# Optimization experiments

Hardware: AMD Instinct MI355X
Metric: run time of the kernel (lower is better)

Reference implementation:

```python
import jax, jax.numpy as jnp
import numpy as np

B, C, T = 1024, 64, 275
S = 10            # number of subjects
EMB = 184         # encoder embedding dim
PROJ = 1024       # projector dim
LN_EPS = 1e-5


def setup_inputs() -> dict:
    key = jax.random.key(0)
    ks = jax.random.split(key, 12)
    sc = lambda *shape: 1.0 / np.sqrt(shape[-1] if len(shape) > 1 else 1.0)
    return {
        "eeg": jax.random.normal(ks[0], (B, C, T), dtype=jnp.float32),
        "subject_ids": jax.random.randint(ks[1], (B,), 0, S, dtype=jnp.int64),
        # per-subject Linear(T, T): y = x @ W.T + b
        "subj_W": jax.random.normal(ks[2], (S, T, T), dtype=jnp.float32) / np.sqrt(T),
        "subj_b": jax.random.normal(ks[3], (S, T), dtype=jnp.float32) * 0.02,
        # encoder stub: flatten (C*T) -> Linear -> EMB
        "enc_W": jax.random.normal(ks[4], (C * T, EMB), dtype=jnp.float32) / np.sqrt(C * T),
        "enc_b": jnp.zeros((EMB,), dtype=jnp.float32),
        # projector: Linear(EMB, PROJ) -> ResidualAdd(GELU -> Linear(PROJ, PROJ)) -> LayerNorm
        "W1": jax.random.normal(ks[5], (EMB, PROJ), dtype=jnp.float32) / np.sqrt(EMB),
        "b1": jnp.zeros((PROJ,), dtype=jnp.float32),
        "W2": jax.random.normal(ks[6], (PROJ, PROJ), dtype=jnp.float32) / np.sqrt(PROJ),
        "b2": jnp.zeros((PROJ,), dtype=jnp.float32),
        "gamma": jnp.ones((PROJ,), dtype=jnp.float32),
        "beta": jnp.zeros((PROJ,), dtype=jnp.float32),
    }


def reference(eeg, subject_ids, subj_W, subj_b, enc_W, enc_b, W1, b1, W2, b2, gamma, beta):
    # --- subject-wise alignment: grouped gather -> linear -> scatter ---
    # Vectorized form of the per-subject loop: each row b uses weight subj_W[sid[b]].
    Wg = subj_W[subject_ids]              # [B, T, T]
    bg = subj_b[subject_ids]              # [B, T]
    # torch Linear: y = x @ W.T + b  ->  y[b,c,u] = sum_t eeg[b,c,t] * Wg[b,u,t]
    x = jnp.einsum("bct,but->bcu", eeg, Wg) + bg[:, None, :]   # [B, C, T]

    # --- encoder stub (SpatioTemporalCNN placeholder): flatten + linear ---
    h = x.reshape(x.shape[0], -1) @ enc_W + enc_b              # [B, EMB]

    # --- MLPProjector ---
    h = h @ W1 + b1                                            # [B, PROJ]
    r = jax.nn.gelu(h, approximate=False) @ W2 + b2            # dropout is identity at eval
    h = h + r
    # LayerNorm over last dim
    mu = jnp.mean(h, axis=-1, keepdims=True)
    var = jnp.mean(jnp.square(h - mu), axis=-1, keepdims=True)
    out = (h - mu) * jax.lax.rsqrt(var + LN_EPS) * gamma + beta
    return out
```

## Files before the change

### kernel.cpp

```cpp
#include <hip/hip_runtime.h>
#include <math.h>

#define B_N    1024
#define C_N    64
#define T_N    275
#define S_N    10
#define EMB_N  184
#define PROJ_N 1024
#define CT_N   (C_N * T_N)
#define TP     288
#define TPAD   296
#define KP2    18432
#define EMBP   192
#define KZ2    32
#define KC2    (KP2 / KZ2)
#define KZ5    2

typedef unsigned short u16;
typedef __attribute__((ext_vector_type(8))) short short8;
typedef __attribute__((ext_vector_type(4))) short short4v;
typedef __attribute__((ext_vector_type(4))) float f32x4;

#define MFMA16(a,b,c) __builtin_amdgcn_mfma_f32_16x16x32_bf16(a, b, c, 0, 0, 0)

__device__ __forceinline__ u16 f2bf(float f) {
    union { float f; unsigned u; } v; v.f = f;
    unsigned r = v.u + 0x7FFFu + ((v.u >> 16) & 1u);
    return (u16)(r >> 16);
}
__device__ __forceinline__ float gelu_exact(float v) {
    return 0.5f * v * (1.0f + erff(v * 0.70710678118654752f));
}
__device__ __forceinline__ void gload16(const void* g, void* lds) {
    __builtin_amdgcn_global_load_lds(
        (const __attribute__((address_space(1))) void*)g,
        (__attribute__((address_space(3))) void*)lds, 16, 0, 0);
}

__global__ __launch_bounds__(256) void p_eeg(const float* __restrict__ eeg,
                                             u16* __restrict__ eegb)
{
    const int b = blockIdx.x;
    const float* src = eeg + (size_t)b * CT_N;
    u16* dst = eegb + (size_t)b * C_N * TPAD;
    for (int o4 = threadIdx.x; o4 < C_N * TPAD / 4; o4 += 256) {
        int o = o4 * 4;
        int r = o / TPAD, tt = o - r * TPAD;
        short4v pk;
        #pragma unroll
        for (int e = 0; e < 4; ++e) {
            int t = tt + e;
            float v = (t < T_N) ? src[r * T_N + t] : 0.f;
            pk[e] = (short)f2bf(v);
        }
        *reinterpret_cast<short4v*>(dst + o) = pk;
    }
}

__global__ __launch_bounds__(256) void p_wbf16(const float* __restrict__ W,
                                               u16* __restrict__ Wb)
{
    int idx4 = blockIdx.x * 256 + threadIdx.x;
    if (idx4 >= S_N * TP * TPAD / 4) return;
    int o = idx4 * 4;
    int row = o / TPAD, tt = o - row * TPAD;
    int s = row / TP, u = row - s * TP;
    short4v pk;
    #pragma unroll
    for (int e = 0; e < 4; ++e) {
        int t = tt + e;
        float v = (u < T_N && t < T_N) ? W[((size_t)s * T_N + u) * T_N + t] : 0.f;
        pk[e] = (short)f2bf(v);
    }
    *reinterpret_cast<short4v*>(Wb + o) = pk;
}

__global__ __launch_bounds__(256) void p_encwt(const float* __restrict__ encW,
                                               u16* __restrict__ eT)
{
    __shared__ float tile[64][65];
    const int t = blockIdx.x;
    const int n0 = blockIdx.y * 64;
    const int tid = threadIdx.x;
    const int j = tid & 63, cg = tid >> 6;
    #pragma unroll
    for (int pass = 0; pass < 16; ++pass) {
        int c = pass * 4 + cg;
        float v = 0.f;
        if (t < T_N && n0 + j < EMB_N)
            v = encW[((size_t)c * T_N + t) * EMB_N + n0 + j];
        tile[c][j] = v;
    }
    __syncthreads();
    #pragma unroll
    for (int pass = 0; pass < 16; ++pass) {
        int nl = pass * 4 + cg;
        eT[(size_t)(n0 + nl) * KP2 + t * 64 + j] = f2bf(tile[j][nl]);
    }
}

__global__ __launch_bounds__(256) void p_w1t(const float* __restrict__ W1,
                                             u16* __restrict__ w1t)
{
    __shared__ float tile[64][65];
    const int k0 = blockIdx.x * 64, n0 = blockIdx.y * 64;
    for (int l = threadIdx.x; l < 4096; l += 256) {
        int i = l >> 6, j = l & 63;
        float v = (k0 + i < EMB_N) ? W1[(size_t)(k0 + i) * PROJ_N + n0 + j] : 0.f;
        tile[i][j] = v;
    }
    __syncthreads();
    for (int l = threadIdx.x; l < 4096; l += 256) {
        int j = l >> 6, i = l & 63;
        w1t[(size_t)(n0 + j) * EMBP + k0 + i] = f2bf(tile[i][j]);
    }
}

__global__ __launch_bounds__(256) void p_w2t(const float* __restrict__ W2,
                                             u16* __restrict__ w2t)
{
    __shared__ float tile[64][65];
    const int k0 = blockIdx.x * 64, n0 = blockIdx.y * 64;
    for (int l = threadIdx.x; l < 4096; l += 256) {
        int i = l >> 6, j = l & 63;
        tile[i][j] = W2[(size_t)(k0 + i) * PROJ_N + n0 + j];
    }
    __syncthreads();
    for (int l = threadIdx.x; l < 4096; l += 256) {
        int j = l >> 6, i = l & 63;
        w2t[(size_t)(n0 + j) * PROJ_N + k0 + i] = f2bf(tile[i][j]);
    }
}

__global__ __launch_bounds__(256) void k1_mfma(
    const u16* __restrict__ eegb, const int* __restrict__ sid,
    const u16* __restrict__ Wb, const float* __restrict__ subj_b,
    u16* __restrict__ xb)
{
    const int b = blockIdx.x;
    const int s = sid[b];
    const int tid = threadIdx.x;
    const int w = tid >> 6, lane = tid & 63;
    const int wr = w >> 1, wc = w & 1;
    const int lrow = lane & 15, lk = lane >> 4;
    const u16* A = eegb + (size_t)b * C_N * TPAD;
    const u16* Wr = Wb + (size_t)s * TP * TPAD;

    f32x4 acc[2][9] = {};
    for (int ks = 0; ks < 9; ++ks) {
        const int t0 = ks * 32 + 8 * lk;
        short8 af0 = *reinterpret_cast<const short8*>(A + (32 * wr + lrow) * TPAD + t0);
        short8 af1 = *reinterpret_cast<const short8*>(A + (32 * wr + 16 + lrow) * TPAD + t0);
        #pragma unroll
        for (int ct = 0; ct < 9; ++ct) {
            int u = 144 * wc + 16 * ct + lrow;
            short8 bf = *reinterpret_cast<const short8*>(Wr + (size_t)u * TPAD + t0);
            acc[0][ct] = MFMA16(af0, bf, acc[0][ct]);
            acc[1][ct] = MFMA16(af1, bf, acc[1][ct]);
        }
    }
    #pragma unroll
    for (int ct = 0; ct < 9; ++ct) {
        int u = 144 * wc + 16 * ct + lrow;
        float bias = (u < T_N) ? subj_b[s * T_N + u] : 0.f;
        bool valid = (u < T_N);
        #pragma unroll
        for (int rt = 0; rt < 2; ++rt) {
            int c0 = 32 * wr + 16 * rt + 4 * lk;
            short4v pk;
            #pragma unroll
            for (int r = 0; r < 4; ++r)
                pk[r] = valid ? (short)f2bf(acc[rt][ct][r] + bias) : (short)0;
            *reinterpret_cast<short4v*>(xb + ((size_t)b * TP + u) * C_N + c0) = pk;
        }
    }
}

__global__ __launch_bounds__(256) void k2_mfma(
    const u16* __restrict__ xb, const u16* __restrict__ eT,
    float* __restrict__ part)
{
    __shared__ u16 Abuf[2][64 * 64];
    const int m0 = blockIdx.x * 64;
    const int kz = blockIdx.y;
    const int tid = threadIdx.x;
    const int w = tid >> 6, lane = tid & 63;
    const int lrow = lane & 15, lk = lane >> 4;
    const int kbase = kz * KC2;

    const int r0 = tid >> 3, q0 = tid & 7;
    const int r1 = (tid + 256) >> 3, q1 = tid & 7;
    const u16* a0 = xb + (size_t)(m0 + r0) * KP2 + (q0 ^ (r0 & 7)) * 8;
    const u16* a1 = xb + (size_t)(m0 + r1) * KP2 + (q1 ^ (r1 & 7)) * 8;

    f32x4 acc[4][3] = {};
    int buf = 0;

    gload16(a0 + kbase, &Abuf[0][(size_t)(w * 64) * 8]);
    gload16(a1 + kbase, &Abuf[0][(size_t)(w * 64 + 256) * 8]);
    __syncthreads();

    for (int step = 0; step < 9; ++step) {
        if (step < 8) {
            int k0 = kbase + (step + 1) * 64;
            gload16(a0 + k0, &Abuf[buf ^ 1][(size_t)(w * 64) * 8]);
            gload16(a1 + k0, &Abuf[buf ^ 1][(size_t)(w * 64 + 256) * 8]);
        }
        short8 bf[3][2];
        #pragma unroll
        for (int ct = 0; ct < 3; ++ct)
            #pragma unroll
            for (int ki = 0; ki < 2; ++ki)
                bf[ct][ki] = *reinterpret_cast<const short8*>(
                    eT + (size_t)(48 * w + 16 * ct + lrow) * KP2 + kbase + step * 64 + ki * 32 + 8 * lk);
        #pragma unroll
        for (int rt = 0; rt < 4; ++rt) {
            int c = 16 * rt + lrow;
            #pragma unroll
            for (int ki = 0; ki < 2; ++ki) {
                short8 af = *reinterpret_cast<const short8*>(
                    &Abuf[buf][c * 64 + (((lk + 4 * ki) ^ (c & 7)) * 8)]);
                #pragma unroll
                for (int ct = 0; ct < 3; ++ct)
                    acc[rt][ct] = MFMA16(af, bf[ct][ki], acc[rt][ct]);
            }
        }
        __syncthreads();
        buf ^= 1;
    }

    #pragma unroll
    for (int rt = 0; rt < 4; ++rt)
        #pragma unroll
        for (int ct = 0; ct < 3; ++ct) {
            int n = 48 * w + 16 * ct + lrow;
            #pragma unroll
            for (int r = 0; r < 4; ++r) {
                int m = m0 + 16 * rt + 4 * lk + r;
                part[((size_t)kz * B_N + m) * EMBP + n] = acc[rt][ct][r];
            }
        }
}

__global__ __launch_bounds__(256) void k3_reduce(
    const float* __restrict__ part, const float* __restrict__ enc_b,
    u16* __restrict__ hb)
{
    int idx = blockIdx.x * 256 + threadIdx.x;
    if (idx >= B_N * EMBP) return;
    int n = idx % EMBP;
    float s = 0.f;
    if (n < EMB_N) {
        s = enc_b[n];
        #pragma unroll
        for (int z = 0; z < KZ2; ++z)
            s += part[(size_t)z * B_N * EMBP + idx];
    }
    hb[idx] = f2bf(s);
}

__global__ __launch_bounds__(256) void k4_mfma(
    const u16* __restrict__ hb, const u16* __restrict__ w1t,
    const float* __restrict__ b1, float* __restrict__ h1, u16* __restrict__ g)
{
    __shared__ u16 Ab[64 * EMBP];
    __shared__ u16 Bb[64 * EMBP];
    const int m0 = blockIdx.x * 64, n0 = blockIdx.y * 64;
    const int tid = threadIdx.x;
    const int w = tid >> 6, lane = tid & 63;
    const int wr = w >> 1, wc = w & 1;
    const int lrow = lane & 15, lk = lane >> 4;

    #pragma unroll
    for (int i = 0; i < 6; ++i) {
        int L = tid + i * 256;
        int row = L / 24, qp = L % 24;
        int ql = qp ^ (row & 7);
        gload16(hb  + (size_t)(m0 + row) * EMBP + ql * 8, &Ab[(size_t)(w * 64 + i * 256) * 8]);
        gload16(w1t + (size_t)(n0 + row) * EMBP + ql * 8, &Bb[(size_t)(w * 64 + i * 256) * 8]);
    }
    __syncthreads();

    f32x4 acc[2][2] = {};
    #pragma unroll
    for (int ks = 0; ks < 6; ++ks) {
        #pragma unroll
        for (int rt = 0; rt < 2; ++rt) {
            int c = 32 * wr + 16 * rt + lrow;
            short8 af = *reinterpret_cast<const short8*>(
                &Ab[c * EMBP + (((4 * ks + lk) ^ (c & 7)) * 8)]);
            #pragma unroll
            for (int ct = 0; ct < 2; ++ct) {
                int nl = 32 * wc + 16 * ct + lrow;
                short8 bfv = *reinterpret_cast<const short8*>(
                    &Bb[nl * EMBP + (((4 * ks + lk) ^ (nl & 7)) * 8)]);
                acc[rt][ct] = MFMA16(af, bfv, acc[rt][ct]);
            }
        }
    }
    #pragma unroll
    for (int rt = 0; rt < 2; ++rt)
        #pragma unroll
        for (int ct = 0; ct < 2; ++ct) {
            int n = n0 + 32 * wc + 16 * ct + lrow;
            #pragma unroll
            for (int r = 0; r < 4; ++r) {
                int m = m0 + 32 * wr + 16 * rt + 4 * lk + r;
                float v = acc[rt][ct][r] + b1[n];
                size_t o = (size_t)m * PROJ_N + n;
                h1[o] = v;
                g[o] = f2bf(gelu_exact(v));
            }
        }
}

__global__ __launch_bounds__(256) void k5_mfma(
    const u16* __restrict__ g, const u16* __restrict__ w2t,
    float* __restrict__ part2)
{
    __shared__ u16 Ab[2][64 * 64];
    __shared__ u16 Bb[2][64 * 64];
    const int m0 = blockIdx.x * 64, n0 = blockIdx.y * 64;
    const int kz = blockIdx.z;
    const int kbase = kz * (PROJ_N / KZ5);
    const int tid = threadIdx.x;
    const int w = tid >> 6, lane = tid & 63;
    const int wr = w >> 1, wc = w & 1;
    const int lrow = lane & 15, lk = lane >> 4;

    const int r0 = tid >> 3, q0 = tid & 7;
    const int r1 = (tid + 256) >> 3;
    const u16* a0 = g + (size_t)(m0 + r0) * PROJ_N + (q0 ^ (r0 & 7)) * 8;
    const u16* a1 = g + (size_t)(m0 + r1) * PROJ_N + (q0 ^ (r1 & 7)) * 8;
    const u16* b0 = w2t + (size_t)(n0 + r0) * PROJ_N + (q0 ^ (r0 & 7)) * 8;
    const u16* b1p = w2t + (size_t)(n0 + r1) * PROJ_N + (q0 ^ (r1 & 7)) * 8;

    f32x4 acc[2][2] = {};
    int buf = 0;
    gload16(a0 + kbase, &Ab[0][(size_t)(w * 64) * 8]);
    gload16(a1 + kbase, &Ab[0][(size_t)(w * 64 + 256) * 8]);
    gload16(b0 + kbase, &Bb[0][(size_t)(w * 64) * 8]);
    gload16(b1p + kbase, &Bb[0][(size_t)(w * 64 + 256) * 8]);
    __syncthreads();

    for (int step = 0; step < 8; ++step) {
        if (step < 7) {
            int k0 = kbase + (step + 1) * 64;
            gload16(a0 + k0, &Ab[buf ^ 1][(size_t)(w * 64) * 8]);
            gload16(a1 + k0, &Ab[buf ^ 1][(size_t)(w * 64 + 256) * 8]);
            gload16(b0 + k0, &Bb[buf ^ 1][(size_t)(w * 64) * 8]);
            gload16(b1p + k0, &Bb[buf ^ 1][(size_t)(w * 64 + 256) * 8]);
        }
        #pragma unroll
        for (int ki = 0; ki < 2; ++ki) {
            #pragma unroll
            for (int rt = 0; rt < 2; ++rt) {
                int c = 32 * wr + 16 * rt + lrow;
                short8 af = *reinterpret_cast<const short8*>(
                    &Ab[buf][c * 64 + (((lk + 4 * ki) ^ (c & 7)) * 8)]);
                #pragma unroll
                for (int ct = 0; ct < 2; ++ct) {
                    int nl = 32 * wc + 16 * ct + lrow;
                    short8 bfv = *reinterpret_cast<const short8*>(
                        &Bb[buf][nl * 64 + (((lk + 4 * ki) ^ (nl & 7)) * 8)]);
                    acc[rt][ct] = MFMA16(af, bfv, acc[rt][ct]);
                }
            }
        }
        __syncthreads();
        buf ^= 1;
    }
    #pragma unroll
    for (int rt = 0; rt < 2; ++rt)
        #pragma unroll
        for (int ct = 0; ct < 2; ++ct) {
            int n = n0 + 32 * wc + 16 * ct + lrow;
            #pragma unroll
            for (int r = 0; r < 4; ++r) {
                int m = m0 + 32 * wr + 16 * rt + 4 * lk + r;
                part2[(size_t)kz * B_N * PROJ_N + (size_t)m * PROJ_N + n] = acc[rt][ct][r];
            }
        }
}

__global__ __launch_bounds__(256) void k5r_ln(
    const float* __restrict__ part2, const float* __restrict__ h1,
    const float* __restrict__ b2, const float* __restrict__ gamma,
    const float* __restrict__ beta, float* __restrict__ out)
{
    const int m = blockIdx.x;
    const int tid = threadIdx.x;
    const float4* h4 = reinterpret_cast<const float4*>(h1 + (size_t)m * PROJ_N);
    const float4* p0 = reinterpret_cast<const float4*>(part2 + (size_t)m * PROJ_N);
    const float4* p1 = reinterpret_cast<const float4*>(part2 + (size_t)(B_N + m) * PROJ_N);
    const float4* b4 = reinterpret_cast<const float4*>(b2);
    float4 va = h4[tid], vb = p0[tid], vc = p1[tid], vd = b4[tid];
    float v[4] = { va.x + vb.x + vc.x + vd.x, va.y + vb.y + vc.y + vd.y,
                   va.z + vb.z + vc.z + vd.z, va.w + vb.w + vc.w + vd.w };
    float s = 0.f, sq = 0.f;
    #pragma unroll
    for (int i = 0; i < 4; ++i) { s += v[i]; sq += v[i] * v[i]; }
    #pragma unroll
    for (int off = 32; off > 0; off >>= 1) {
        s  += __shfl_down(s, off);
        sq += __shfl_down(sq, off);
    }
    __shared__ float ss[4], ssq[4];
    int wid = tid >> 6, lane = tid & 63;
    if (lane == 0) { ss[wid] = s; ssq[wid] = sq; }
    __syncthreads();
    if (tid == 0) {
        float a = 0.f, bsum = 0.f;
        #pragma unroll
        for (int q = 0; q < 4; ++q) { a += ss[q]; bsum += ssq[q]; }
        ss[0] = a; ssq[0] = bsum;
    }
    __syncthreads();
    float mu  = ss[0] * (1.0f / PROJ_N);
    float var = ssq[0] * (1.0f / PROJ_N) - mu * mu;
    float rs  = rsqrtf(var + 1e-5f);
    const float4 g4 = reinterpret_cast<const float4*>(gamma)[tid];
    const float4 be4 = reinterpret_cast<const float4*>(beta)[tid];
    float gg[4] = { g4.x, g4.y, g4.z, g4.w };
    float bb[4] = { be4.x, be4.y, be4.z, be4.w };
    float4 o4;
    float* op = reinterpret_cast<float*>(&o4);
    #pragma unroll
    for (int i = 0; i < 4; ++i) op[i] = (v[i] - mu) * rs * gg[i] + bb[i];
    reinterpret_cast<float4*>(out + (size_t)m * PROJ_N)[tid] = o4;
}

extern "C" void kernel_launch(void* const* d_in, const int* in_sizes, int n_in,
                              void* d_out, int out_size, void* d_ws, size_t ws_size,
                              hipStream_t stream)
{
    const float* eeg    = (const float*)d_in[0];
    const int*   sid    = (const int*)  d_in[1];
    const float* subj_W = (const float*)d_in[2];
    const float* subj_b = (const float*)d_in[3];
    const float* enc_W  = (const float*)d_in[4];
    const float* enc_b  = (const float*)d_in[5];
    const float* W1     = (const float*)d_in[6];
    const float* b1     = (const float*)d_in[7];
    const float* W2     = (const float*)d_in[8];
    const float* b2     = (const float*)d_in[9];
    const float* gamma  = (const float*)d_in[10];
    const float* beta   = (const float*)d_in[11];
    float* out = (float*)d_out;

    char* w = (char*)d_ws;
    u16*   xb    = (u16*)(w);
    u16*   Wb    = (u16*)(w + 37748736);
    u16*   eT    = (u16*)(w + 39453696);
    u16*   w1t   = (u16*)(w + 46531584);
    u16*   w2t   = (u16*)(w + 46924800);
    u16*   hb    = (u16*)(w + 49021952);
    float* h1    = (float*)(w + 49415168);
    u16*   g     = (u16*)(w + 53609472);
    char*  scr   = w + 55706624;
    u16*   eegb  = (u16*)scr;
    float* part  = (float*)scr;
    float* part2 = (float*)(scr + 25165824);

    p_eeg   <<<dim3(B_N), 256, 0, stream>>>(eeg, eegb);
    p_wbf16 <<<dim3((S_N * TP * TPAD / 4 + 255) / 256), 256, 0, stream>>>(subj_W, Wb);
    p_encwt <<<dim3(TP, 3), 256, 0, stream>>>(enc_W, eT);
    p_w1t   <<<dim3(EMBP / 64, PROJ_N / 64), 256, 0, stream>>>(W1, w1t);
    p_w2t   <<<dim3(PROJ_N / 64, PROJ_N / 64), 256, 0, stream>>>(W2, w2t);

    k1_mfma <<<dim3(B_N), 256, 0, stream>>>(eegb, sid, Wb, subj_b, xb);
    k2_mfma <<<dim3(16, KZ2), 256, 0, stream>>>(xb, eT, part);
    k3_reduce<<<dim3((B_N * EMBP + 255) / 256), 256, 0, stream>>>(part, enc_b, hb);
    k4_mfma <<<dim3(16, 16), 256, 0, stream>>>(hb, w1t, b1, h1, g);
    k5_mfma <<<dim3(16, 16, KZ5), 256, 0, stream>>>(g, w2t, part2);
    k5r_ln  <<<dim3(B_N), 256, 0, stream>>>(part2, h1, b2, gamma, beta, out);
}
```

Before: 143.2 us.

## Fuse prep kernels, group batches by subject in k1, enlarge k2 tile

Merges the five preprocessing kernels into one launch and adds a block that buckets batch rows by subject id into groups of four. The subject-wise GEMM then processes four same-subject rows per 512-thread block, staging the shared subject weight in double-buffered LDS so it is reused across rows. The encoder GEMM tile grows to 128 rows with register prefetch of the B operand, and the TPAD padding is removed. These changes aim to cut launch overhead and redundant weight traffic, in exchange for more registers, padded groups that do no useful work, and a serial prefix computation inside the fused prep kernel.

After: 132.2 us. 1.08x faster.

```diff
diff --git a/kernel.cpp b/kernel.cpp
--- a/kernel.cpp
+++ b/kernel.cpp
@@ -9,12 +9,12 @@
 #define PROJ_N 1024
 #define CT_N   (C_N * T_N)
 #define TP     288
-#define TPAD   296
-#define KP2    18432
+#define KP2    (TP * C_N)
 #define EMBP   192
 #define KZ2    32
 #define KC2    (KP2 / KZ2)
 #define KZ5    2
+#define GMAX   264
 
 typedef unsigned short u16;
 typedef __attribute__((ext_vector_type(8))) short short8;
@@ -37,200 +37,290 @@
         (__attribute__((address_space(3))) void*)lds, 16, 0, 0);
 }
 
-__global__ __launch_bounds__(256) void p_eeg(const float* __restrict__ eeg,
-                                             u16* __restrict__ eegb)
-{
-    const int b = blockIdx.x;
-    const float* src = eeg + (size_t)b * CT_N;
-    u16* dst = eegb + (size_t)b * C_N * TPAD;
-    for (int o4 = threadIdx.x; o4 < C_N * TPAD / 4; o4 += 256) {
-        int o = o4 * 4;
-        int r = o / TPAD, tt = o - r * TPAD;
+__global__ __launch_bounds__(256) void p_all(
+    const float* __restrict__ eeg, const int* __restrict__ sid,
+    const float* __restrict__ W, const float* __restrict__ encW,
+    const float* __restrict__ W1, const float* __restrict__ W2,
+    u16* __restrict__ eegb, u16* __restrict__ Wb, u16* __restrict__ eT,
+    u16* __restrict__ w1t, u16* __restrict__ w2t, int* __restrict__ bsq)
+{
+    __shared__ char smem[16640];
+    const int blk = blockIdx.x;
+    const int tid = threadIdx.x;
+
+    if (blk < 1024) {
+        const int b = blk;
+        const float* src = eeg + (size_t)b * CT_N;
+        u16* dst = eegb + (size_t)b * C_N * TP;
+        #pragma unroll
+        for (int p = 0; p < 9; ++p) {
+            int ch = tid + p * 256;
+            int c = ch / 36, q8 = ch - c * 36;
+            int t0 = q8 * 8;
+            short8 pk;
+            #pragma unroll
+            for (int e = 0; e < 8; ++e) {
+                int t = t0 + e;
+                float v = (t < T_N) ? src[c * T_N + t] : 0.f;
+                pk[e] = (short)f2bf(v);
+            }
+            *reinterpret_cast<short8*>(dst + c * TP + t0) = pk;
+        }
+        return;
+    }
+    if (blk < 1834) {
+        int idx4 = (blk - 1024) * 256 + tid;
+        if (idx4 >= S_N * TP * TP / 4) return;
+        int o = idx4 * 4;
+        int row = o / TP, t = o - row * TP;
+        int s = row / TP, u = row - s * TP;
         short4v pk;
         #pragma unroll
         for (int e = 0; e < 4; ++e) {
-            int t = tt + e;
-            float v = (t < T_N) ? src[r * T_N + t] : 0.f;
+            float v = (u < T_N && t + e < T_N)
+                ? W[((size_t)s * T_N + u) * T_N + t + e] : 0.f;
             pk[e] = (short)f2bf(v);
         }
-        *reinterpret_cast<short4v*>(dst + o) = pk;
-    }
-}
-
-__global__ __launch_bounds__(256) void p_wbf16(const float* __restrict__ W,
-                                               u16* __restrict__ Wb)
-{
-    int idx4 = blockIdx.x * 256 + threadIdx.x;
-    if (idx4 >= S_N * TP * TPAD / 4) return;
-    int o = idx4 * 4;
-    int row = o / TPAD, tt = o - row * TPAD;
-    int s = row / TP, u = row - s * TP;
-    short4v pk;
-    #pragma unroll
-    for (int e = 0; e < 4; ++e) {
-        int t = tt + e;
-        float v = (u < T_N && t < T_N) ? W[((size_t)s * T_N + u) * T_N + t] : 0.f;
-        pk[e] = (short)f2bf(v);
-    }
-    *reinterpret_cast<short4v*>(Wb + o) = pk;
-}
-
-__global__ __launch_bounds__(256) void p_encwt(const float* __restrict__ encW,
-                                               u16* __restrict__ eT)
-{
-    __shared__ float tile[64][65];
-    const int t = blockIdx.x;
-    const int n0 = blockIdx.y * 64;
-    const int tid = threadIdx.x;
-    const int j = tid & 63, cg = tid >> 6;
-    #pragma unroll
-    for (int pass = 0; pass < 16; ++pass) {
-        int c = pass * 4 + cg;
-        float v = 0.f;
-        if (t < T_N && n0 + j < EMB_N)
-            v = encW[((size_t)c * T_N + t) * EMB_N + n0 + j];
-        tile[c][j] = v;
-    }
-    __syncthreads();
-    #pragma unroll
-    for (int pass = 0; pass < 16; ++pass) {
-        int nl = pass * 4 + cg;
-        eT[(size_t)(n0 + nl) * KP2 + t * 64 + j] = f2bf(tile[j][nl]);
-    }
-}
-
-__global__ __launch_bounds__(256) void p_w1t(const float* __restrict__ W1,
-                                             u16* __restrict__ w1t)
-{
-    __shared__ float tile[64][65];
-    const int k0 = blockIdx.x * 64, n0 = blockIdx.y * 64;
-    for (int l = threadIdx.x; l < 4096; l += 256) {
-        int i = l >> 6, j = l & 63;
-        float v = (k0 + i < EMB_N) ? W1[(size_t)(k0 + i) * PROJ_N + n0 + j] : 0.f;
-        tile[i][j] = v;
-    }
-    __syncthreads();
-    for (int l = threadIdx.x; l < 4096; l += 256) {
-        int j = l >> 6, i = l & 63;
-        w1t[(size_t)(n0 + j) * EMBP + k0 + i] = f2bf(tile[i][j]);
-    }
-}
-
-__global__ __launch_bounds__(256) void p_w2t(const float* __restrict__ W2,
-                                             u16* __restrict__ w2t)
-{
-    __shared__ float tile[64][65];
-    const int k0 = blockIdx.x * 64, n0 = blockIdx.y * 64;
-    for (int l = threadIdx.x; l < 4096; l += 256) {
-        int i = l >> 6, j = l & 63;
-        tile[i][j] = W2[(size_t)(k0 + i) * PROJ_N + n0 + j];
-    }
-    __syncthreads();
-    for (int l = threadIdx.x; l < 4096; l += 256) {
-        int j = l >> 6, i = l & 63;
-        w2t[(size_t)(n0 + j) * PROJ_N + k0 + i] = f2bf(tile[i][j]);
-    }
-}
-
-__global__ __launch_bounds__(256) void k1_mfma(
+        *reinterpret_cast<short4v*>(Wb + o) = pk;
+        return;
+    }
+    if (blk < 2698) {
+        float (*tile)[65] = (float(*)[65])smem;
+        int local = blk - 1834;
+        const int t = local / 3;
+        const int n0 = (local % 3) * 64;
+        const int j = tid & 63, cg = tid >> 6;
+        #pragma unroll
+        for (int pass = 0; pass < 16; ++pass) {
+            int c = pass * 4 + cg;
+            float v = 0.f;
+            if (t < T_N && n0 + j < EMB_N)
+                v = encW[((size_t)c * T_N + t) * EMB_N + n0 + j];
+            tile[c][j] = v;
+        }
+        __syncthreads();
+        #pragma unroll
+        for (int pass = 0; pass < 16; ++pass) {
+            int nl = pass * 4 + cg;
+            eT[(size_t)(n0 + nl) * KP2 + t * 64 + j] = f2bf(tile[j][nl]);
+        }
+        return;
+    }
+    if (blk < 2746) {
+        float (*tile)[65] = (float(*)[65])smem;
+        int local = blk - 2698;
+        const int k0 = (local % 3) * 64, n0 = (local / 3) * 64;
+        for (int l = tid; l < 4096; l += 256) {
+            int i = l >> 6, j = l & 63;
+            float v = (k0 + i < EMB_N) ? W1[(size_t)(k0 + i) * PROJ_N + n0 + j] : 0.f;
+            tile[i][j] = v;
+        }
+        __syncthreads();
+        for (int l = tid; l < 4096; l += 256) {
+            int j = l >> 6, i = l & 63;
+            w1t[(size_t)(n0 + j) * EMBP + k0 + i] = f2bf(tile[i][j]);
+        }
+        return;
+    }
+    if (blk < 3002) {
+        float (*tile)[65] = (float(*)[65])smem;
+        int local = blk - 2746;
+        const int k0 = (local % 16) * 64, n0 = (local / 16) * 64;
+        for (int l = tid; l < 4096; l += 256) {
+            int i = l >> 6, j = l & 63;
+            tile[i][j] = W2[(size_t)(k0 + i) * PROJ_N + n0 + j];
+        }
+        __syncthreads();
+        for (int l = tid; l < 4096; l += 256) {
+            int j = l >> 6, i = l & 63;
+            w2t[(size_t)(n0 + j) * PROJ_N + k0 + i] = f2bf(tile[i][j]);
+        }
+        return;
+    }
+    {
+        int* sgrp = (int*)smem;
+        int* C    = (int*)(smem + 4096);
+        int* tot  = (int*)(smem + 4096 + 640);
+        for (int i = tid; i < 1024; i += 256) sgrp[i] = sid[i];
+        for (int i = tid; i < 4 * GMAX; i += 256) bsq[i] = -1;
+        __syncthreads();
+        const int w4 = tid >> 6, lane = tid & 63;
+        #pragma unroll
+        for (int j = 0; j < 4; ++j) {
+            int chunk = w4 * 4 + j;
+            int sb = sgrp[chunk * 64 + lane];
+            int myc = 0;
+            for (int s = 0; s < S_N; ++s) {
+                unsigned long long m = __ballot(sb == s);
+                if (lane == s) myc = (int)__popcll(m);
+            }
+            if (lane < S_N) C[chunk * S_N + lane] = myc;
+        }
+        __syncthreads();
+        if (tid < S_N) {
+            int a = 0;
+            for (int w2 = 0; w2 < 16; ++w2) a += C[w2 * S_N + tid];
+            tot[tid] = a;
+        }
+        __syncthreads();
+        #pragma unroll
+        for (int rep = 0; rep < 4; ++rep) {
+            int b = tid + rep * 256;
+            int s = sgrp[b];
+            int off = 0;
+            for (int s2 = 0; s2 < S_N; ++s2)
+                if (s2 < s) off += (tot[s2] + 3) & ~3;
+            int chunk = b >> 6;
+            int rank = 0;
+            for (int w2 = 0; w2 < 16; ++w2)
+                if (w2 < chunk) rank += C[w2 * S_N + s];
+            for (int i = chunk * 64; i < b; ++i) rank += (sgrp[i] == s) ? 1 : 0;
+            bsq[off + rank] = b;
+        }
+    }
+}
+
+__global__ __launch_bounds__(512, 2) void k1g(
     const u16* __restrict__ eegb, const int* __restrict__ sid,
     const u16* __restrict__ Wb, const float* __restrict__ subj_b,
-    u16* __restrict__ xb)
-{
-    const int b = blockIdx.x;
-    const int s = sid[b];
+    const int* __restrict__ bsq, u16* __restrict__ xb)
+{
+    __shared__ u16 Bs[2][TP * 4 * 8];
+    const int g = blockIdx.x;
+    const int b0 = bsq[g * 4];
+    if (b0 < 0) return;
+    const int s = sid[b0];
     const int tid = threadIdx.x;
     const int w = tid >> 6, lane = tid & 63;
-    const int wr = w >> 1, wc = w & 1;
+    const int bi = w >> 1, uh = w & 1;
     const int lrow = lane & 15, lk = lane >> 4;
-    const u16* A = eegb + (size_t)b * C_N * TPAD;
-    const u16* Wr = Wb + (size_t)s * TP * TPAD;
-
-    f32x4 acc[2][9] = {};
+    const int b = bsq[g * 4 + bi];
+    const int bsafe = (b >= 0) ? b : 0;
+    const u16* A = eegb + (size_t)bsafe * C_N * TP;
+    const u16* Wr = Wb + (size_t)s * TP * TP;
+
+    #define K1_STAGE(st, ks)                                                   \
+        for (int l = tid; l < TP * 4; l += 512) {                              \
+            int u_ = l >> 2, q_ = l & 3;                                       \
+            gload16(Wr + (size_t)u_ * TP + (ks) * 32 + ((q_ ^ ((u_ >> 1) & 3)) << 3), \
+                    &Bs[st][l * 8]);                                           \
+        }
+
+    f32x4 acc[4][9] = {};
+    short8 a[4], an[4];
+
+    K1_STAGE(0, 0);
+    #pragma unroll
+    for (int rt = 0; rt < 4; ++rt)
+        a[rt] = *reinterpret_cast<const short8*>(A + (16 * rt + lrow) * TP + 8 * lk);
+    __syncthreads();
+
     for (int ks = 0; ks < 9; ++ks) {
-        const int t0 = ks * 32 + 8 * lk;
-        short8 af0 = *reinterpret_cast<const short8*>(A + (32 * wr + lrow) * TPAD + t0);
-        short8 af1 = *reinterpret_cast<const short8*>(A + (32 * wr + 16 + lrow) * TPAD + t0);
+        const int st = ks & 1;
+        if (ks < 8) {
+            K1_STAGE(st ^ 1, ks + 1);
+            #pragma unroll
+            for (int rt = 0; rt < 4; ++rt)
+                an[rt] = *reinterpret_cast<const short8*>(
+                    A + (16 * rt + lrow) * TP + (ks + 1) * 32 + 8 * lk);
+        }
         #pragma unroll
         for (int ct = 0; ct < 9; ++ct) {
-            int u = 144 * wc + 16 * ct + lrow;
-            short8 bf = *reinterpret_cast<const short8*>(Wr + (size_t)u * TPAD + t0);
-            acc[0][ct] = MFMA16(af0, bf, acc[0][ct]);
-            acc[1][ct] = MFMA16(af1, bf, acc[1][ct]);
-        }
-    }
+            int u = uh * 144 + 16 * ct + lrow;
+            int chunk = u * 4 + (lk ^ ((u >> 1) & 3));
+            short8 bv = *reinterpret_cast<const short8*>(&Bs[st][chunk * 8]);
+            #pragma unroll
+            for (int rt = 0; rt < 4; ++rt)
+                acc[rt][ct] = MFMA16(a[rt], bv, acc[rt][ct]);
+        }
+        __syncthreads();
+        #pragma unroll
+        for (int rt = 0; rt < 4; ++rt) a[rt] = an[rt];
+    }
+
+    if (b < 0) return;
     #pragma unroll
     for (int ct = 0; ct < 9; ++ct) {
-        int u = 144 * wc + 16 * ct + lrow;
-        float bias = (u < T_N) ? subj_b[s * T_N + u] : 0.f;
-        bool valid = (u < T_N);
-        #pragma unroll
-        for (int rt = 0; rt < 2; ++rt) {
-            int c0 = 32 * wr + 16 * rt + 4 * lk;
+        int u = uh * 144 + 16 * ct + lrow;
+        if (u >= T_N) continue;
+        float bias = subj_b[s * T_N + u];
+        #pragma unroll
+        for (int rt = 0; rt < 4; ++rt) {
+            int c0 = 16 * rt + 4 * lk;
             short4v pk;
             #pragma unroll
             for (int r = 0; r < 4; ++r)
-                pk[r] = valid ? (short)f2bf(acc[rt][ct][r] + bias) : (short)0;
+                pk[r] = (short)f2bf(acc[rt][ct][r] + bias);
             *reinterpret_cast<short4v*>(xb + ((size_t)b * TP + u) * C_N + c0) = pk;
         }
     }
+    #undef K1_STAGE
 }
 
 __global__ __launch_bounds__(256) void k2_mfma(
     const u16* __restrict__ xb, const u16* __restrict__ eT,
     float* __restrict__ part)
 {
-    __shared__ u16 Abuf[2][64 * 64];
-    const int m0 = blockIdx.x * 64;
+    __shared__ u16 Ab[2][128 * 64];
+    const int m0 = blockIdx.x * 128;
     const int kz = blockIdx.y;
+    const int kbase = kz * KC2;
     const int tid = threadIdx.x;
     const int w = tid >> 6, lane = tid & 63;
     const int lrow = lane & 15, lk = lane >> 4;
-    const int kbase = kz * KC2;
-
-    const int r0 = tid >> 3, q0 = tid & 7;
-    const int r1 = (tid + 256) >> 3, q1 = tid & 7;
-    const u16* a0 = xb + (size_t)(m0 + r0) * KP2 + (q0 ^ (r0 & 7)) * 8;
-    const u16* a1 = xb + (size_t)(m0 + r1) * KP2 + (q1 ^ (r1 & 7)) * 8;
-
-    f32x4 acc[4][3] = {};
-    int buf = 0;
-
-    gload16(a0 + kbase, &Abuf[0][(size_t)(w * 64) * 8]);
-    gload16(a1 + kbase, &Abuf[0][(size_t)(w * 64 + 256) * 8]);
+
+    #define K2_STAGE(st, step)                                                 \
+        _Pragma("unroll")                                                      \
+        for (int p = 0; p < 4; ++p) {                                          \
+            int l = tid + p * 256;                                             \
+            int r_ = l >> 3, q_ = l & 7;                                       \
+            gload16(xb + (size_t)(m0 + r_) * KP2 + kbase + (step) * 64 +       \
+                        ((q_ ^ (r_ & 7)) << 3),                                \
+                    &Ab[st][l * 8]);                                           \
+        }
+
+    #define K2_BLOAD(step, dst)                                                \
+        _Pragma("unroll")                                                      \
+        for (int ct = 0; ct < 3; ++ct)                                         \
+            _Pragma("unroll")                                                  \
+            for (int ki = 0; ki < 2; ++ki)                                     \
+                dst[ct][ki] = *reinterpret_cast<const short8*>(                \
+                    eT + (size_t)(48 * w + 16 * ct + lrow) * KP2 + kbase +     \
+                    (step) * 64 + ki * 32 + 8 * lk);
+
+    f32x4 acc[8][3] = {};
+    short8 bf[3][2], bn[3][2];
+
+    K2_STAGE(0, 0);
+    K2_BLOAD(0, bf);
     __syncthreads();
 
     for (int step = 0; step < 9; ++step) {
+        const int st = step & 1;
         if (step < 8) {
-            int k0 = kbase + (step + 1) * 64;
-            gload16(a0 + k0, &Abuf[buf ^ 1][(size_t)(w * 64) * 8]);
-            gload16(a1 + k0, &Abuf[buf ^ 1][(size_t)(w * 64 + 256) * 8]);
-        }
-        short8 bf[3][2];
-        #pragma unroll
-        for (int ct = 0; ct < 3; ++ct)
-            #pragma unroll
-            for (int ki = 0; ki < 2; ++ki)
-                bf[ct][ki] = *reinterpret_cast<const short8*>(
-                    eT + (size_t)(48 * w + 16 * ct + lrow) * KP2 + kbase + step * 64 + ki * 32 + 8 * lk);
-        #pragma unroll
-        for (int rt = 0; rt < 4; ++rt) {
-            int c = 16 * rt + lrow;
-            #pragma unroll
-            for (int ki = 0; ki < 2; ++ki) {
-                short8 af = *reinterpret_cast<const short8*>(
-                    &Abuf[buf][c * 64 + (((lk + 4 * ki) ^ (c & 7)) * 8)]);
+            K2_STAGE(st ^ 1, step + 1);
+            K2_BLOAD(step + 1, bn);
+        }
+        #pragma unroll
+        for (int ki = 0; ki < 2; ++ki)
+            #pragma unroll
+            for (int rt = 0; rt < 8; ++rt) {
+                int m = 16 * rt + lrow;
+                int chunk = m * 8 + ((4 * ki + lk) ^ (m & 7));
+                short8 af = *reinterpret_cast<const short8*>(&Ab[st][chunk * 8]);
                 #pragma unroll
                 for (int ct = 0; ct < 3; ++ct)
                     acc[rt][ct] = MFMA16(af, bf[ct][ki], acc[rt][ct]);
             }
-        }
-        __syncthreads();
-        buf ^= 1;
-    }
-
-    #pragma unroll
-    for (int rt = 0; rt < 4; ++rt)
+        __syncthreads();
+        #pragma unroll
+        for (int ct = 0; ct < 3; ++ct)
+            #pragma unroll
+            for (int ki = 0; ki < 2; ++ki) bf[ct][ki] = bn[ct][ki];
+    }
+
+    #pragma unroll
+    for (int rt = 0; rt < 8; ++rt)
         #pragma unroll
         for (int ct = 0; ct < 3; ++ct) {
             int n = 48 * w + 16 * ct + lrow;
@@ -240,6 +330,8 @@
                 part[((size_t)kz * B_N + m) * EMBP + n] = acc[rt][ct][r];
             }
         }
+    #undef K2_STAGE
+    #undef K2_BLOAD
 }
 
 __global__ __launch_bounds__(256) void k3_reduce(
@@ -276,8 +368,8 @@
         int L = tid + i * 256;
         int row = L / 24, qp = L % 24;
         int ql = qp ^ (row & 7);
-        gload16(hb  + (size_t)(m0 + row) * EMBP + ql * 8, &Ab[(size_t)(w * 64 + i * 256) * 8]);
-        gload16(w1t + (size_t)(n0 + row) * EMBP + ql * 8, &Bb[(size_t)(w * 64 + i * 256) * 8]);
+        gload16(hb  + (size_t)(m0 + row) * EMBP + ql * 8, &Ab[(size_t)L * 8]);
+        gload16(w1t + (size_t)(n0 + row) * EMBP + ql * 8, &Bb[(size_t)L * 8]);
     }
     __syncthreads();
 
@@ -451,27 +543,24 @@
     char* w = (char*)d_ws;
     u16*   xb    = (u16*)(w);
     u16*   Wb    = (u16*)(w + 37748736);
-    u16*   eT    = (u16*)(w + 39453696);
-    u16*   w1t   = (u16*)(w + 46531584);
-    u16*   w2t   = (u16*)(w + 46924800);
-    u16*   hb    = (u16*)(w + 49021952);
-    float* h1    = (float*)(w + 49415168);
-    u16*   g     = (u16*)(w + 53609472);
-    char*  scr   = w + 55706624;
+    u16*   eT    = (u16*)(w + 39407616);
+    u16*   w1t   = (u16*)(w + 46485504);
+    u16*   w2t   = (u16*)(w + 46878720);
+    u16*   hb    = (u16*)(w + 48975872);
+    float* h1    = (float*)(w + 49369088);
+    u16*   g     = (u16*)(w + 53563392);
+    int*   bsq   = (int*)(w + 55660544);
+    char*  scr   = w + 55664896;
     u16*   eegb  = (u16*)scr;
     float* part  = (float*)scr;
     float* part2 = (float*)(scr + 25165824);
 
-    p_eeg   <<<dim3(B_N), 256, 0, stream>>>(eeg, eegb);
-    p_wbf16 <<<dim3((S_N * TP * TPAD / 4 + 255) / 256), 256, 0, stream>>>(subj_W, Wb);
-    p_encwt <<<dim3(TP, 3), 256, 0, stream>>>(enc_W, eT);
-    p_w1t   <<<dim3(EMBP / 64, PROJ_N / 64), 256, 0, stream>>>(W1, w1t);
-    p_w2t   <<<dim3(PROJ_N / 64, PROJ_N / 64), 256, 0, stream>>>(W2, w2t);
-
-    k1_mfma <<<dim3(B_N), 256, 0, stream>>>(eegb, sid, Wb, subj_b, xb);
-    k2_mfma <<<dim3(16, KZ2), 256, 0, stream>>>(xb, eT, part);
+    p_all<<<dim3(3003), 256, 0, stream>>>(eeg, sid, subj_W, enc_W, W1, W2,
+                                          eegb, Wb, eT, w1t, w2t, bsq);
+    k1g  <<<dim3(GMAX), 512, 0, stream>>>(eegb, sid, Wb, subj_b, bsq, xb);
+    k2_mfma<<<dim3(8, KZ2), 256, 0, stream>>>(xb, eT, part);
     k3_reduce<<<dim3((B_N * EMBP + 255) / 256), 256, 0, stream>>>(part, enc_b, hb);
-    k4_mfma <<<dim3(16, 16), 256, 0, stream>>>(hb, w1t, b1, h1, g);
-    k5_mfma <<<dim3(16, 16, KZ5), 256, 0, stream>>>(g, w2t, part2);
-    k5r_ln  <<<dim3(B_N), 256, 0, stream>>>(part2, h1, b2, gamma, beta, out);
-}
+    k4_mfma<<<dim3(16, 16), 256, 0, stream>>>(hb, w1t, b1, h1, g);
+    k5_mfma<<<dim3(16, 16, KZ5), 256, 0, stream>>>(g, w2t, part2);
+    k5r_ln <<<dim3(B_N), 256, 0, stream>>>(part2, h1, b2, gamma, beta, out);
+}
```
